# Kernel tuning notes

Measured on AMD Instinct MI355X. Metric: run time of the kernel, lower is better.

## Reference

```python
import jax, jax.numpy as jnp
import numpy as np
from jax import lax

T, B, H, NF, FS = 512, 128, 512, 128, 5  # max_seq_len, batch, hidden, num_filters, filter_size


def setup_inputs() -> dict:
    key = jax.random.key(0)
    ks = jax.random.split(key, 16)
    inp = {
        "encoder_output": jax.random.normal(ks[0], (T, B, H), dtype=jnp.float32),
        "lengths": jax.random.randint(ks[1], (B,), 1, T + 1, dtype=jnp.int64 if jax.config.jax_enable_x64 else jnp.int32),
    }
    for w in range(1, FS + 1):
        inp[f"conv_w{w}"] = jax.random.normal(ks[1 + w], (NF, 1, H, w), dtype=jnp.float32) * 0.02
        inp[f"conv_b{w}"] = jnp.zeros((NF,), dtype=jnp.float32)
    inp["fc1_w"] = jax.random.normal(ks[12], (100, FS * NF), dtype=jnp.float32) * 0.05
    inp["fc1_b"] = jnp.zeros((100,), dtype=jnp.float32)
    inp["fc2_w"] = jax.random.normal(ks[13], (1, 100), dtype=jnp.float32) * 0.1
    inp["fc2_b"] = jnp.zeros((1,), dtype=jnp.float32)
    return inp


def _raw_reshape(x, L):
    # Faithful to torch .contiguous().view(1,1,H,-1) on a [L,H] slice:
    # row-major flatten of first L rows, reshaped to [H, L], zero-padded to [H, T].
    flat = x.reshape(-1)                       # [T*H]
    h = jnp.arange(H)[:, None]                 # [H,1]
    l = jnp.arange(T)[None, :]                 # [1,T]
    return jnp.where(l < L, flat[h * L + l], 0.0)  # [H,T]


def reference(encoder_output, lengths,
              conv_w1, conv_b1, conv_w2, conv_b2, conv_w3, conv_b3,
              conv_w4, conv_b4, conv_w5, conv_b5,
              fc1_w, fc1_b, fc2_w, fc2_b):
    # encoder_output: [T, B, H]; per-sample raw reshape to [H, T] (length-dependent)
    X = jax.vmap(_raw_reshape, in_axes=(1, 0))(encoder_output, lengths)  # [B,H,T]
    X4 = X[:, None, :, :]                                               # [B,1,H,T]
    Leff = jnp.maximum(lengths, FS)  # torch code zero-pads width to >= filter_size
    conv_ws = [conv_w1, conv_w2, conv_w3, conv_w4, conv_w5]
    conv_bs = [conv_b1, conv_b2, conv_b3, conv_b4, conv_b5]
    pools = []
    for w in range(1, FS + 1):
        out = lax.conv_general_dilated(
            X4, conv_ws[w - 1], window_strides=(1, 1), padding='VALID',
            dimension_numbers=('NCHW', 'OIHW', 'NCHW'))          # [B,NF,1,T-w+1]
        r = jax.nn.relu(out[:, :, 0, :] + conv_bs[w - 1][None, :, None])  # [B,NF,Tw]
        tpos = jnp.arange(T - w + 1)
        valid = tpos[None, :] < (Leff - w + 1)[:, None]          # [B,Tw]
        r = jnp.where(valid[:, None, :], r, 0.0)                 # relu>=0, so 0 is safe for max
        pools.append(r.max(axis=2))                              # [B,NF]
    feat = jnp.concatenate(pools, axis=1)                        # [B,FS*NF]
    fc1 = feat @ fc1_w.T + fc1_b
    fc2 = fc1 @ fc2_w.T + fc2_b
    probs = jax.nn.sigmoid(fc2)                                  # [B,1]
    return probs[:, None, :]                                     # [B,1,1] == torch.stack of [1,1]
```

## Files before the change

kernel.cpp:

```cpp
#include <hip/hip_runtime.h>
#include <hip/hip_bf16.h>

#define TT 512
#define BB 128
#define HH 512
#define NFC 128

typedef short v8s __attribute__((ext_vector_type(8)));
typedef float v4f __attribute__((ext_vector_type(4)));

__device__ __forceinline__ unsigned short f2bf(float x) {
    unsigned u = __float_as_uint(x);
    unsigned r = (u + 0x7fffu + ((u >> 16) & 1u)) >> 16;
    return (unsigned short)r;
}

__global__ void prep_all(const float* __restrict__ enc, const int* __restrict__ lengths,
                         unsigned short* __restrict__ Xg,
                         const float* __restrict__ w1, const float* __restrict__ w2,
                         const float* __restrict__ w3, const float* __restrict__ w4,
                         const float* __restrict__ w5, unsigned short* __restrict__ Wg,
                         float* __restrict__ pools,
                         const float* __restrict__ fc1w, const float* __restrict__ fc1b,
                         const float* __restrict__ fc2w, const float* __restrict__ fc2b,
                         float* __restrict__ v, int* __restrict__ wl) {
    int blk = blockIdx.x;
    int tid = threadIdx.x;
    if (blk < 8192) {
        __shared__ float tile[64 * 65];
        int b = blk >> 6;
        int lc = (blk >> 3) & 7;
        int hc = blk & 7;
        int L = lengths[b];
        int Leff = L > 5 ? L : 5;
        int l0 = lc * 64, h0 = hc * 64;
        if (l0 >= Leff + 127) return;
        int lx = tid & 63;
        int hq = tid >> 6;
        #pragma unroll
        for (int r = 0; r < 16; ++r) {
            int hl = hq * 16 + r;
            int l = l0 + lx;
            float val = 0.f;
            if (l < L) {
                int i = (h0 + hl) * L + l;
                val = enc[(i >> 9) * (BB * HH) + b * HH + (i & 511)];
            }
            tile[hl * 65 + lx] = val;
        }
        __syncthreads();
        int hg = tid & 15;
        #pragma unroll
        for (int r = 0; r < 4; ++r) {
            int lloc = (tid >> 4) + r * 16;
            int n = b * 512 + l0 + lloc;
            ushort4 pk;
            pk.x = f2bf(tile[(hg * 4 + 0) * 65 + lloc]);
            pk.y = f2bf(tile[(hg * 4 + 1) * 65 + lloc]);
            pk.z = f2bf(tile[(hg * 4 + 2) * 65 + lloc]);
            pk.w = f2bf(tile[(hg * 4 + 3) * 65 + lloc]);
            *(ushort4*)&Xg[n * 512 + h0 + hg * 4] = pk;
        }
    } else if (blk < 12288) {
        int idx = (blk - 8192) * 256 + tid;
        int s = idx >> 9, h = idx & 511;
        int f = s >> 4, sl = s & 15;
        float val = 0.f;
        if (sl < 15) {
            int w, j;
            if (sl < 1)       { w = 1; j = sl; }
            else if (sl < 3)  { w = 2; j = sl - 1; }
            else if (sl < 6)  { w = 3; j = sl - 3; }
            else if (sl < 10) { w = 4; j = sl - 6; }
            else              { w = 5; j = sl - 10; }
            const float* wp = (w == 1) ? w1 : (w == 2) ? w2 : (w == 3) ? w3 : (w == 4) ? w4 : w5;
            val = wp[f * (HH * w) + h * w + j];
        }
        Wg[idx] = f2bf(val);
    } else if (blk < 12608) {
        int i = (blk - 12288) * 256 + tid;
        if (i < BB * 5 * NFC) pools[i] = 0.f;
    } else if (blk == 12608) {
        for (int k = tid; k < 640; k += 256) {
            float s = 0.f;
            for (int o = 0; o < 100; ++o) s += fc2w[o] * fc1w[o * 640 + k];
            v[k] = s;
        }
        if (tid == 0) {
            float c = fc2b[0];
            for (int o = 0; o < 100; ++o) c += fc2w[o] * fc1b[o];
            v[640] = c;
        }
    } else {
        __shared__ int cnt;
        if (tid == 0) cnt = 0;
        __syncthreads();
        for (int it = tid; it < 640; it += 256) {
            int b = it / 5, tt = it % 5;
            int L = lengths[b];
            int Leff = L > 5 ? L : 5;
            int n0 = tt * 124 - ((tt >> 2) * 112);
            if (n0 < Leff) {
                int pos = atomicAdd(&cnt, 1);
                wl[pos] = (b << 3) | tt;
            }
        }
        __syncthreads();
        if (tid == 0) wl[640] = cnt;
    }
}

__global__ __launch_bounds__(256, 4)
void conv_gemm(const unsigned short* __restrict__ Wg, const unsigned short* __restrict__ Xg,
               const int* __restrict__ lengths, const int* __restrict__ wl,
               const float* __restrict__ cb1, const float* __restrict__ cb2,
               const float* __restrict__ cb3, const float* __restrict__ cb4,
               const float* __restrict__ cb5,
               float* __restrict__ pools) {
    __shared__ __align__(16) char smem[64 * 129 * 4];
    unsigned short* ldsA = (unsigned short*)smem;
    unsigned short* ldsB = (unsigned short*)(smem + 16384);
    float* Gs = (float*)smem;

    int cnt = wl[640];
    int wk = blockIdx.y;
    if (wk >= cnt) return;
    int item = wl[wk];
    int b = item >> 3, tt = item & 7;
    int mt = blockIdx.x;
    int n0 = tt * 124 - ((tt >> 2) * 112);
    int L = lengths[b];
    int Leff = L > 5 ? L : 5;

    int tid = threadIdx.x;
    int wid = tid >> 6, lane = tid & 63;
    int wm = wid >> 1, wn = wid & 1;
    int llo = lane & 15, quad = lane >> 4;
    int psw = quad ^ ((llo >> 1) & 3);

    int m0 = mt * 128;
    int nb0 = b * 512 + n0;

    v4f acc[4][4];
    #pragma unroll
    for (int i = 0; i < 4; ++i)
        #pragma unroll
        for (int j = 0; j < 4; ++j) acc[i][j] = v4f{0.f, 0.f, 0.f, 0.f};

    int srow = lane >> 2;
    int gchunk = (lane & 3) ^ ((lane >> 3) & 3);
    const unsigned short* gA = Wg + (m0 + wid * 32 + srow) * 512 + gchunk * 8;
    const unsigned short* gB = Xg + (nb0 + wid * 32 + srow) * 512 + gchunk * 8;
    int sdst = (wid * 32) * 32;

    #pragma unroll
    for (int q = 0; q < 2; ++q) {
        __builtin_amdgcn_global_load_lds(
            (const __attribute__((address_space(1))) unsigned int*)(gA + q * (16 * 512)),
            (__attribute__((address_space(3))) unsigned int*)&ldsA[sdst + q * 512],
            16, 0, 0);
        __builtin_amdgcn_global_load_lds(
            (const __attribute__((address_space(1))) unsigned int*)(gB + q * (16 * 512)),
            (__attribute__((address_space(3))) unsigned int*)&ldsB[sdst + q * 512],
            16, 0, 0);
    }
    __syncthreads();

    #pragma unroll 1
    for (int kt = 0; kt < 16; ++kt) {
        if (kt < 15) {
            int ko = (kt + 1) * 32;
            int bb = ((kt + 1) & 1) * 4096;
            #pragma unroll
            for (int q = 0; q < 2; ++q) {
                __builtin_amdgcn_global_load_lds(
                    (const __attribute__((address_space(1))) unsigned int*)(gA + q * (16 * 512) + ko),
                    (__attribute__((address_space(3))) unsigned int*)&ldsA[bb + sdst + q * 512],
                    16, 0, 0);
                __builtin_amdgcn_global_load_lds(
                    (const __attribute__((address_space(1))) unsigned int*)(gB + q * (16 * 512) + ko),
                    (__attribute__((address_space(3))) unsigned int*)&ldsB[bb + sdst + q * 512],
                    16, 0, 0);
            }
        }
        int boff = (kt & 1) * 4096;
        v8s Af[4], Bf[4];
        #pragma unroll
        for (int mi = 0; mi < 4; ++mi)
            Af[mi] = *(const v8s*)&ldsA[boff + (wm * 64 + mi * 16 + llo) * 32 + psw * 8];
        #pragma unroll
        for (int ni = 0; ni < 4; ++ni)
            Bf[ni] = *(const v8s*)&ldsB[boff + (wn * 64 + ni * 16 + llo) * 32 + psw * 8];
        #pragma unroll
        for (int mi = 0; mi < 4; ++mi)
            #pragma unroll
            for (int ni = 0; ni < 4; ++ni)
                acc[mi][ni] = __builtin_amdgcn_mfma_f32_16x16x32_bf16(Af[mi], Bf[ni], acc[mi][ni], 0, 0, 0);
        __syncthreads();
    }

    const int basew[6] = {0, 0, 1, 3, 6, 10};

    #pragma unroll
    for (int phase = 0; phase < 2; ++phase) {
        if (wm == phase) {
            #pragma unroll
            for (int mi = 0; mi < 4; ++mi)
                #pragma unroll
                for (int ni = 0; ni < 4; ++ni)
                    #pragma unroll
                    for (int r = 0; r < 4; ++r)
                        Gs[(mi * 16 + quad * 4 + r) * 129 + wn * 64 + ni * 16 + llo] = acc[mi][ni][r];
        }
        __syncthreads();
        {
            int fl = wid;
            int f = mt * 8 + phase * 4 + fl;
            #pragma unroll
            for (int w = 1; w <= 5; ++w) {
                float bias = (w == 1 ? cb1 : w == 2 ? cb2 : w == 3 ? cb3 : w == 4 ? cb4 : cb5)[f];
                int limv = Leff - w + 1 - n0;
                float vmax = -1.f;
                #pragma unroll
                for (int half = 0; half < 2; ++half) {
                    int t = half * 64 + lane;
                    if (t <= 128 - w && t < limv) {
                        float s = 0.f;
                        #pragma unroll
                        for (int j = 0; j < w; ++j)
                            s += Gs[(fl * 16 + basew[w] + j) * 129 + t + j];
                        s += bias;
                        s = fmaxf(s, 0.f);
                        vmax = fmaxf(vmax, s);
                    }
                }
                #pragma unroll
                for (int off = 32; off >= 1; off >>= 1)
                    vmax = fmaxf(vmax, __shfl_xor(vmax, off));
                if (lane == 0 && vmax >= 0.f)
                    atomicMax((int*)&pools[(b * 5 + (w - 1)) * NFC + f], __float_as_int(vmax));
            }
        }
        __syncthreads();
    }
}

__global__ void head(const float* __restrict__ pools, const float* __restrict__ v,
                     float* __restrict__ out) {
    int b = blockIdx.x;
    int tid = threadIdx.x;
    float s = 0.f;
    for (int k = tid; k < 640; k += 256) s += pools[b * 640 + k] * v[k];
    __shared__ float red[256];
    red[tid] = s;
    __syncthreads();
    for (int st = 128; st; st >>= 1) {
        if (tid < st) red[tid] += red[tid + st];
        __syncthreads();
    }
    if (tid == 0) out[b] = 1.f / (1.f + expf(-(red[0] + v[640])));
}

extern "C" void kernel_launch(void* const* d_in, const int* in_sizes, int n_in,
                              void* d_out, int out_size, void* d_ws, size_t ws_size,
                              hipStream_t stream) {
    const float* enc  = (const float*)d_in[0];
    const int* lens   = (const int*)d_in[1];
    const float* w1   = (const float*)d_in[2];
    const float* b1   = (const float*)d_in[3];
    const float* w2   = (const float*)d_in[4];
    const float* b2   = (const float*)d_in[5];
    const float* w3   = (const float*)d_in[6];
    const float* b3   = (const float*)d_in[7];
    const float* w4   = (const float*)d_in[8];
    const float* b4   = (const float*)d_in[9];
    const float* w5   = (const float*)d_in[10];
    const float* b5   = (const float*)d_in[11];
    const float* fc1w = (const float*)d_in[12];
    const float* fc1b = (const float*)d_in[13];
    const float* fc2w = (const float*)d_in[14];
    const float* fc2b = (const float*)d_in[15];
    float* out = (float*)d_out;

    unsigned short* Xg = (unsigned short*)d_ws;
    unsigned short* Wg = Xg + 33554432;
    float* pools  = (float*)(Wg + 1048576);
    float* vbuf   = pools + 81920;
    int* wlist    = (int*)(vbuf + 641);

    prep_all<<<12610, 256, 0, stream>>>(enc, lens, Xg, w1, w2, w3, w4, w5, Wg, pools,
                                        fc1w, fc1b, fc2w, fc2b, vbuf, wlist);
    conv_gemm<<<dim3(16, 640), 256, 0, stream>>>(Wg, Xg, lens, wlist, b1, b2, b3, b4, b5, pools);
    head<<<128, 256, 0, stream>>>(pools, vbuf, out);
}
```

Baseline: 374.2 us.

## Triple-buffer conv GEMM LDS tiles with prefetch depth two and explicit waitcnts

Moves the conv GEMM K-loop from double to triple buffering in LDS, prefetching two K-tiles ahead. It replaces __syncthreads with explicit vmcnt waits and split barriers around the LDS fragment reads, and raises wave priority during the MFMA block. The aim is to hide global-to-LDS load latency behind compute. In exchange, LDS use grows to 48KB and the launch-bounds occupancy hint drops from 4 to 3 blocks per CU.

```diff
diff --git a/kernel.cpp b/kernel.cpp
--- a/kernel.cpp
+++ b/kernel.cpp
@@ -110,16 +110,16 @@
     }
 }
 
-__global__ __launch_bounds__(256, 4)
+__global__ __launch_bounds__(256, 3)
 void conv_gemm(const unsigned short* __restrict__ Wg, const unsigned short* __restrict__ Xg,
                const int* __restrict__ lengths, const int* __restrict__ wl,
                const float* __restrict__ cb1, const float* __restrict__ cb2,
                const float* __restrict__ cb3, const float* __restrict__ cb4,
                const float* __restrict__ cb5,
                float* __restrict__ pools) {
-    __shared__ __align__(16) char smem[64 * 129 * 4];
+    __shared__ __align__(16) char smem[49152];
     unsigned short* ldsA = (unsigned short*)smem;
-    unsigned short* ldsB = (unsigned short*)(smem + 16384);
+    unsigned short* ldsB = ldsA + 12288;
     float* Gs = (float*)smem;
 
     int cnt = wl[640];
@@ -154,36 +154,46 @@
     int sdst = (wid * 32) * 32;
 
     #pragma unroll
-    for (int q = 0; q < 2; ++q) {
-        __builtin_amdgcn_global_load_lds(
-            (const __attribute__((address_space(1))) unsigned int*)(gA + q * (16 * 512)),
-            (__attribute__((address_space(3))) unsigned int*)&ldsA[sdst + q * 512],
-            16, 0, 0);
-        __builtin_amdgcn_global_load_lds(
-            (const __attribute__((address_space(1))) unsigned int*)(gB + q * (16 * 512)),
-            (__attribute__((address_space(3))) unsigned int*)&ldsB[sdst + q * 512],
-            16, 0, 0);
-    }
-    __syncthreads();
-
+    for (int p = 0; p < 2; ++p) {
+        #pragma unroll
+        for (int q = 0; q < 2; ++q) {
+            __builtin_amdgcn_global_load_lds(
+                (const __attribute__((address_space(1))) unsigned int*)(gA + q * (16 * 512) + p * 32),
+                (__attribute__((address_space(3))) unsigned int*)&ldsA[p * 4096 + sdst + q * 512],
+                16, 0, 0);
+            __builtin_amdgcn_global_load_lds(
+                (const __attribute__((address_space(1))) unsigned int*)(gB + q * (16 * 512) + p * 32),
+                (__attribute__((address_space(3))) unsigned int*)&ldsB[p * 4096 + sdst + q * 512],
+                16, 0, 0);
+        }
+    }
+
+    int bcur = 0;
     #pragma unroll 1
     for (int kt = 0; kt < 16; ++kt) {
-        if (kt < 15) {
-            int ko = (kt + 1) * 32;
-            int bb = ((kt + 1) & 1) * 4096;
+        if (kt < 14) {
+            int bnx = bcur + 2; if (bnx >= 3) bnx -= 3;
+            int ko = (kt + 2) * 32;
             #pragma unroll
             for (int q = 0; q < 2; ++q) {
                 __builtin_amdgcn_global_load_lds(
                     (const __attribute__((address_space(1))) unsigned int*)(gA + q * (16 * 512) + ko),
-                    (__attribute__((address_space(3))) unsigned int*)&ldsA[bb + sdst + q * 512],
+                    (__attribute__((address_space(3))) unsigned int*)&ldsA[bnx * 4096 + sdst + q * 512],
                     16, 0, 0);
                 __builtin_amdgcn_global_load_lds(
                     (const __attribute__((address_space(1))) unsigned int*)(gB + q * (16 * 512) + ko),
-                    (__attribute__((address_space(3))) unsigned int*)&ldsB[bb + sdst + q * 512],
+                    (__attribute__((address_space(3))) unsigned int*)&ldsB[bnx * 4096 + sdst + q * 512],
                     16, 0, 0);
             }
-        }
-        int boff = (kt & 1) * 4096;
+            asm volatile("s_waitcnt vmcnt(8)" ::: "memory");
+        } else if (kt == 14) {
+            asm volatile("s_waitcnt vmcnt(4)" ::: "memory");
+        } else {
+            asm volatile("s_waitcnt vmcnt(0)" ::: "memory");
+        }
+        __builtin_amdgcn_s_barrier();
+
+        int boff = bcur * 4096;
         v8s Af[4], Bf[4];
         #pragma unroll
         for (int mi = 0; mi < 4; ++mi)
@@ -191,12 +201,19 @@
         #pragma unroll
         for (int ni = 0; ni < 4; ++ni)
             Bf[ni] = *(const v8s*)&ldsB[boff + (wn * 64 + ni * 16 + llo) * 32 + psw * 8];
+        asm volatile("s_waitcnt lgkmcnt(0)" ::: "memory");
+        __builtin_amdgcn_sched_barrier(0);
+        __builtin_amdgcn_s_barrier();
+
+        __builtin_amdgcn_s_setprio(1);
         #pragma unroll
         for (int mi = 0; mi < 4; ++mi)
             #pragma unroll
             for (int ni = 0; ni < 4; ++ni)
                 acc[mi][ni] = __builtin_amdgcn_mfma_f32_16x16x32_bf16(Af[mi], Bf[ni], acc[mi][ni], 0, 0, 0);
-        __syncthreads();
+        __builtin_amdgcn_s_setprio(0);
+
+        bcur += 1; if (bcur >= 3) bcur -= 3;
     }
 
     const int basew[6] = {0, 0, 1, 3, 6, 10};
```

Result: no change. 381.4 us (+1.9%).
